# Kernel tuning notes

Measured on AMD Instinct MI355X. Metric: run time of the kernel, lower is better.

## Reference

```python
import jax, jax.numpy as jnp
import numpy as np

B = 64       # number of graphs
R = 148      # fixed ROI count from source
D = 64       # hidden_channels (embed_dim, 4 heads)
H = 4
IN1 = 64     # node feature dim (after stripping label column)
INR = 148    # roi-graph feature dim
HID = 1000
NCLS = 2
N1 = 262144
E1 = 1048576
N2 = B * R
E2 = 262144
EPS = 1e-5


def setup_inputs() -> dict:
    key = jax.random.key(0)
    ks = jax.random.split(key, 40)
    def p(i, shape, s=0.1):
        return jax.random.normal(ks[i], shape, dtype=jnp.float32) * s
    inp = {
        'x_feat': jax.random.normal(ks[0], (N1, IN1), dtype=jnp.float32),
        'node_roi': jax.random.randint(ks[1], (N1,), 0, R, dtype=jnp.int32),
        'batch1': ((jnp.arange(N1, dtype=jnp.int32) * B) // N1).astype(jnp.int32),
        'edge_index1': jax.random.randint(ks[2], (2, E1), 0, N1, dtype=jnp.int32),
        'edge_weight1': jax.random.uniform(ks[3], (E1,), dtype=jnp.float32, minval=0.1, maxval=1.0),
        'x2_feat': jax.random.normal(ks[4], (N2, INR), dtype=jnp.float32),
        'roi_labels2': (jnp.arange(N2, dtype=jnp.int32) % R).astype(jnp.int32),
        'batch2': (jnp.arange(N2, dtype=jnp.int32) // R).astype(jnp.int32),
        'edge_index2': jax.random.randint(ks[5], (2, E2), 0, N2, dtype=jnp.int32),
        'edge_weight2': jax.random.uniform(ks[6], (E2,), dtype=jnp.float32, minval=0.1, maxval=1.0),
        'Wg1': p(7, (IN1, D)), 'bg1': jnp.zeros((D,), jnp.float32),
        'Wg2': p(8, (D, D)), 'bg2': jnp.zeros((D,), jnp.float32),
        'Wr1': p(9, (INR, D)), 'br1': jnp.zeros((D,), jnp.float32),
        'Wr2': p(10, (D, D)), 'br2': jnp.zeros((D,), jnp.float32),
        'in_proj_w': p(11, (3 * D, D)), 'in_proj_b': jnp.zeros((3 * D,), jnp.float32),
        'out_proj_w': p(12, (D, D)), 'out_proj_b': jnp.zeros((D,), jnp.float32),
        'ln1_g': jnp.ones((D,), jnp.float32), 'ln1_b': jnp.zeros((D,), jnp.float32),
        'ff_w1': p(13, (D, D)), 'ff_b1': jnp.zeros((D,), jnp.float32),
        'ff_w2': p(14, (D, D)), 'ff_b2': jnp.zeros((D,), jnp.float32),
        'ln2_g': jnp.ones((D,), jnp.float32), 'ln2_b': jnp.zeros((D,), jnp.float32),
        'Wc1': p(15, (R * D, HID), 0.02), 'bc1': jnp.zeros((HID,), jnp.float32),
        'bn_g': jnp.ones((HID,), jnp.float32), 'bn_b': jnp.zeros((HID,), jnp.float32),
        'Wc2': p(16, (HID, NCLS), 0.02), 'bc2': jnp.zeros((NCLS,), jnp.float32),
    }
    return inp


def gcn_conv(h, src, dst, ew, W, b, n):
    # PyG GCNConv w/ edge weights: add self-loops (weight 1), sym-normalize.
    h = h @ W
    deg = jax.ops.segment_sum(ew, dst, num_segments=n) + 1.0
    dinv = jax.lax.rsqrt(deg)
    norm = dinv[src] * ew * dinv[dst]                      # (E,)
    agg = jax.ops.segment_sum(h[src] * norm[:, None], dst, num_segments=n)
    agg = agg + h * (dinv * dinv)[:, None]                 # self-loop term
    return agg + b


def roi_pool_mean(h, roi, batch):
    # fused scatter mean keyed by (batch, roi) -> (B, R, d); empty slots stay 0
    seg = batch * R + roi
    sums = jax.ops.segment_sum(h, seg, num_segments=B * R)
    cnt = jax.ops.segment_sum(jnp.ones_like(h[:, 0]), seg, num_segments=B * R)
    return (sums / jnp.maximum(cnt, 1.0)[:, None]).reshape(B, R, h.shape[1])


def layer_norm(x, g, b):
    mu = x.mean(axis=-1, keepdims=True)
    var = x.var(axis=-1, keepdims=True)
    return (x - mu) * jax.lax.rsqrt(var + EPS) * g + b


def reference(x_feat, node_roi, batch1, edge_index1, edge_weight1,
              x2_feat, roi_labels2, batch2, edge_index2, edge_weight2,
              Wg1, bg1, Wg2, bg2, Wr1, br1, Wr2, br2,
              in_proj_w, in_proj_b, out_proj_w, out_proj_b,
              ln1_g, ln1_b, ff_w1, ff_b1, ff_w2, ff_b2, ln2_g, ln2_b,
              Wc1, bc1, bn_g, bn_b, Wc2, bc2):
    s1, d1 = edge_index1[0], edge_index1[1]
    s2, d2 = edge_index2[0], edge_index2[1]

    # ROI-graph branch (convs_roi[:-1]): 2 GCN layers, relu, eval dropout=noop
    h2 = jax.nn.relu(gcn_conv(x2_feat, s2, d2, edge_weight2, Wr1, br1, N2))
    h2 = jax.nn.relu(gcn_conv(h2, s2, d2, edge_weight2, Wr2, br2, N2))
    pooled_roi = roi_pool_mean(h2, roi_labels2, batch2)          # (B,R,D)

    # node-graph branch (convs[:-1])
    h1 = jax.nn.relu(gcn_conv(x_feat, s1, d1, edge_weight1, Wg1, bg1, N1))
    h1 = jax.nn.relu(gcn_conv(h1, s1, d1, edge_weight1, Wg2, bg2, N1))
    pooled = roi_pool_mean(h1, node_roi, batch1)                 # (B,R,D)

    combined = pooled + pooled_roi                               # transformer_in_combined

    # SelfAttnBlock (torch MultiheadAttention, batch_first, 4 heads)
    hd = D // H
    qkv = combined @ in_proj_w.T + in_proj_b                     # (B,R,3D)
    q, k, v = jnp.split(qkv, 3, axis=-1)
    q = q.reshape(B, R, H, hd)
    k = k.reshape(B, R, H, hd)
    v = v.reshape(B, R, H, hd)
    scores = jnp.einsum('bqhd,bkhd->bhqk', q, k) / np.sqrt(hd).astype(np.float32)
    attn_w = jax.nn.softmax(scores, axis=-1)                     # (B,H,R,R)
    o = jnp.einsum('bhqk,bkhd->bqhd', attn_w, v).reshape(B, R, D)
    o = o @ out_proj_w.T + out_proj_b
    x = layer_norm(combined + o, ln1_g, ln1_b)
    f = jax.nn.relu(x @ ff_w1 + ff_b1) @ ff_w2 + ff_b2
    t_out = layer_norm(x + f, ln2_g, ln2_b)                      # (B,R,D)

    # classifier: Linear -> BatchNorm1d(eval: mean0,var1) -> LeakyReLU -> Linear
    z = t_out.reshape(B, R * D) @ Wc1 + bc1
    z = bn_g * z * jax.lax.rsqrt(jnp.asarray(1.0 + EPS, z.dtype)) + bn_b
    z = jnp.where(z >= 0, z, 0.01 * z)
    out = z @ Wc2 + bc2                                          # (B,NCLS)
    return (out, pooled, pooled_roi, t_out, attn_w)
```

## Files before the change

kernel.cpp:

```cpp
#include <hip/hip_runtime.h>
#include <cstdint>
#include <cstddef>

#define N1v 262144
#define E1v 1048576
#define N2v 9472
#define E2v 262144
#define BBv 64
#define RRv 148
#define HIDv 1000
#define BRv (BBv * RRv)
#define NSEG 9472
#define EPB 4096
#define NBK1 256
#define SH1 10
#define BINS1 1024
#define CAP1 4864
#define STR1 4608
#define NBK2 74
#define SH2 7
#define BINS2 128
#define CAP2 4096
#define STR2 4096
#define GB1 4096
#define GB2 1184
#define MB1 2048
#define MB2 148
#define PH_B2 (E1v / EPB + E2v / EPB)
#define PH_G1 MB1
#define PH_PC BBv
#define PH_TR 64

__host__ __device__ constexpr int cdiv(int a, int b) { return (a + b - 1) / b; }

typedef __attribute__((ext_vector_type(8))) short bf16x8;
typedef __attribute__((ext_vector_type(4))) float f32x4;
typedef unsigned short ushort_t;
typedef unsigned long long u64;

__device__ inline short f2bf(float f) {
    union { float f; unsigned u; } v; v.f = f;
    unsigned r = v.u + 0x7fff + ((v.u >> 16) & 1);
    return (short)(r >> 16);
}
__device__ inline float bf2f(unsigned hs) {
    union { unsigned u; float f; } v; v.u = hs << 16; return v.f;
}
__device__ inline unsigned relu_pk(unsigned u) {
    unsigned r = u;
    if (r & 0x8000u) r &= 0xFFFF0000u;
    if (r & 0x80000000u) r &= 0x0000FFFFu;
    return r;
}

__device__ inline void binB2_body(const int* __restrict__ src, const int* __restrict__ dst,
                                  const float* __restrict__ ew, int* __restrict__ cur, u64* __restrict__ rb,
                                  int nbk, int sh, int e0, size_t stride,
                                  int* __restrict__ h, int* __restrict__ basg) {
    int tid = threadIdx.x;
    if (tid < nbk) h[tid] = 0;
    __syncthreads();
    for (int t = tid; t < EPB; t += 256) atomicAdd(&h[dst[e0 + t] >> sh], 1);
    __syncthreads();
    if (tid < nbk) {
        int c = h[tid];
        basg[tid] = c ? atomicAdd(&cur[tid], c) : 0;
        h[tid] = 0;
    }
    __syncthreads();
    unsigned lowmask = (1u << sh) - 1u;
    for (int t = tid; t < EPB; t += 256) {
        int d = dst[e0 + t];
        int b = d >> sh;
        int r = atomicAdd(&h[b], 1);
        unsigned lo = ((unsigned)src[e0 + t] << sh) | ((unsigned)d & lowmask);
        rb[(size_t)b * stride + basg[b] + r] = ((u64)(unsigned)__float_as_int(ew[e0 + t]) << 32) | lo;
    }
}

__device__ inline void gemm_f32_body(const float* __restrict__ X, const float* __restrict__ Wmat,
                                     ushort_t* __restrict__ Y, int N, int gw, int tw, int tid) {
    int lane = tid & 63;
    int l15 = lane & 15;
    int lg = lane >> 4;
    bf16x8 bfrag[2][4];
    for (int kh = 0; kh < 2; ++kh)
        for (int ct = 0; ct < 4; ++ct) {
            bf16x8 b;
#pragma unroll
            for (int i = 0; i < 8; ++i)
                b[i] = f2bf(Wmat[(size_t)(kh * 32 + lg * 8 + i) * 64 + ct * 16 + l15]);
            bfrag[kh][ct] = b;
        }
    int ntiles = N >> 4;
    for (int t = gw; t < ntiles; t += tw) {
        int row0 = t << 4;
        const float* xp = X + (size_t)(row0 + l15) * 64 + lg * 8;
        float4 a0 = *(const float4*)(xp);
        float4 a1 = *(const float4*)(xp + 4);
        float4 a2 = *(const float4*)(xp + 32);
        float4 a3 = *(const float4*)(xp + 36);
        bf16x8 af0, af1;
        af0[0] = f2bf(a0.x); af0[1] = f2bf(a0.y); af0[2] = f2bf(a0.z); af0[3] = f2bf(a0.w);
        af0[4] = f2bf(a1.x); af0[5] = f2bf(a1.y); af0[6] = f2bf(a1.z); af0[7] = f2bf(a1.w);
        af1[0] = f2bf(a2.x); af1[1] = f2bf(a2.y); af1[2] = f2bf(a2.z); af1[3] = f2bf(a2.w);
        af1[4] = f2bf(a3.x); af1[5] = f2bf(a3.y); af1[6] = f2bf(a3.z); af1[7] = f2bf(a3.w);
        f32x4 acc0 = {0.f, 0.f, 0.f, 0.f}, acc1 = acc0, acc2 = acc0, acc3 = acc0;
        acc0 = __builtin_amdgcn_mfma_f32_16x16x32_bf16(af0, bfrag[0][0], acc0, 0, 0, 0);
        acc1 = __builtin_amdgcn_mfma_f32_16x16x32_bf16(af0, bfrag[0][1], acc1, 0, 0, 0);
        acc2 = __builtin_amdgcn_mfma_f32_16x16x32_bf16(af0, bfrag[0][2], acc2, 0, 0, 0);
        acc3 = __builtin_amdgcn_mfma_f32_16x16x32_bf16(af0, bfrag[0][3], acc3, 0, 0, 0);
        acc0 = __builtin_amdgcn_mfma_f32_16x16x32_bf16(af1, bfrag[1][0], acc0, 0, 0, 0);
        acc1 = __builtin_amdgcn_mfma_f32_16x16x32_bf16(af1, bfrag[1][1], acc1, 0, 0, 0);
        acc2 = __builtin_amdgcn_mfma_f32_16x16x32_bf16(af1, bfrag[1][2], acc2, 0, 0, 0);
        acc3 = __builtin_amdgcn_mfma_f32_16x16x32_bf16(af1, bfrag[1][3], acc3, 0, 0, 0);
        ushort_t* yp = Y + (size_t)(row0 + lg * 4) * 64 + l15;
#pragma unroll
        for (int r = 0; r < 4; ++r) {
            yp[(size_t)r * 64 + 0]  = (ushort_t)f2bf(acc0[r]);
            yp[(size_t)r * 64 + 16] = (ushort_t)f2bf(acc1[r]);
            yp[(size_t)r * 64 + 32] = (ushort_t)f2bf(acc2[r]);
            yp[(size_t)r * 64 + 48] = (ushort_t)f2bf(acc3[r]);
        }
    }
}

__device__ inline void pool_csr_body(const int* __restrict__ roi, int* __restrict__ offs_p,
                                     int* __restrict__ nodeC, int b, int* __restrict__ smem) {
    int* rl = smem;
    int* hist = smem + 4096;
    int* curs = smem + 4096 + RRv;
    int tid = threadIdx.x;
    for (int t = tid; t < RRv; t += 256) hist[t] = 0;
    __syncthreads();
    int base = b * 4096;
    for (int t = tid; t < 4096; t += 256) {
        int r = roi[base + t];
        rl[t] = r;
        atomicAdd(&hist[r], 1);
    }
    __syncthreads();
    if (tid < RRv) {
        int s = 0;
        for (int k = 0; k < tid; ++k) s += hist[k];
        curs[tid] = s;
        offs_p[b * RRv + tid] = base + s;
    }
    __syncthreads();
    for (int t = tid; t < 4096; t += 256) {
        int r = rl[t];
        int j = atomicAdd(&curs[r], 1);
        nodeC[base + j] = base + t;
    }
}

__global__ __launch_bounds__(256) void k_phase1(
    const int* __restrict__ src1, const int* __restrict__ dst1, const float* __restrict__ ew1,
    int* __restrict__ cur1, u64* __restrict__ rb1,
    const int* __restrict__ src2, const int* __restrict__ dst2, const float* __restrict__ ew2,
    int* __restrict__ cur2, u64* __restrict__ rb2,
    const float* __restrict__ x_feat, const float* __restrict__ Wg1, ushort_t* __restrict__ h1P,
    const int* __restrict__ roi, int* __restrict__ offs_p, int* __restrict__ nodeC,
    const float* __restrict__ Win, float* __restrict__ WinT,
    const float* __restrict__ Wout, float* __restrict__ WoutT) {
    __shared__ int smem[4096 + 2 * RRv];
    int bid = blockIdx.x;
    int tid = threadIdx.x;
    if (bid < PH_B2) {
        if (bid < E1v / EPB)
            binB2_body(src1, dst1, ew1, cur1, rb1, NBK1, SH1, bid * EPB, STR1, smem, smem + 256);
        else
            binB2_body(src2, dst2, ew2, cur2, rb2, NBK2, SH2, (bid - E1v / EPB) * EPB, STR2, smem, smem + 256);
    } else if (bid < PH_B2 + PH_G1) {
        gemm_f32_body(x_feat, Wg1, h1P, N1v, (bid - PH_B2) * 4 + (tid >> 6), PH_G1 * 4, tid);
    } else if (bid < PH_B2 + PH_G1 + PH_PC) {
        pool_csr_body(roi, offs_p, nodeC, bid - PH_B2 - PH_G1, smem);
    } else {
        int i = (bid - PH_B2 - PH_G1 - PH_PC) * 256 + tid;
        if (i < 192 * 64) {
            WinT[(i & 63) * 192 + (i >> 6)] = Win[i];
        } else if (i < 192 * 64 + 64 * 64) {
            int j = i - 192 * 64;
            WoutT[(j & 63) * 64 + (j >> 6)] = Wout[j];
        }
    }
}

__global__ __launch_bounds__(256) void k_scanC(const int* __restrict__ cur1, int* __restrict__ cb1,
                                               const int* __restrict__ cur2, int* __restrict__ cb2) {
    __shared__ int tmp[256];
    int t = threadIdx.x;
    int v = cur1[t];
    tmp[t] = v; __syncthreads();
    int val = v;
    for (int off = 1; off < 256; off <<= 1) { int o = (t >= off) ? tmp[t - off] : 0; __syncthreads(); val += o; tmp[t] = val; __syncthreads(); }
    cb1[t] = val - v;
    if (t == 255) cb1[256] = val;
    __syncthreads();
    int v2 = (t < NBK2) ? cur2[t] : 0;
    tmp[t] = v2; __syncthreads();
    int val2 = v2;
    for (int off = 1; off < 256; off <<= 1) { int o = (t >= off) ? tmp[t - off] : 0; __syncthreads(); val2 += o; tmp[t] = val2; __syncthreads(); }
    if (t < NBK2) cb2[t] = val2 - v2;
    if (t == NBK2 - 1) cb2[NBK2] = val2;
}

template<int BINS, int CAP, int SH, int STRIDE>
__global__ __launch_bounds__(256) void k_csrC(const u64* __restrict__ rb, const int* __restrict__ cnts,
                                              const int* __restrict__ cbase,
                                              float* __restrict__ dinv, int* __restrict__ offs,
                                              int2* __restrict__ snC) {
    int b = blockIdx.x;
    const u64* rbb = rb + (size_t)b * STRIDE;
    int cnt = cnts[b];
    int cb = cbase[b];
    __shared__ int hist[BINS];
    __shared__ float degs[BINS];
    __shared__ int scn[BINS];
    __shared__ int tmp[256];
    extern __shared__ int2 outb[];
    int tid = threadIdx.x;
    for (int i = tid; i < BINS; i += 256) { hist[i] = 0; degs[i] = 0.f; }
    __syncthreads();
    for (int j = tid; j < cnt; j += 256) {
        u64 rec = rbb[j];
        int bin = (int)((unsigned)rec & (BINS - 1));
        float w = __int_as_float((int)(rec >> 32));
        atomicAdd(&hist[bin], 1);
        atomicAdd(&degs[bin], w);
    }
    __syncthreads();
    constexpr int PER = (BINS + 255) / 256;
    int lv[PER];
    int tsum = 0;
    int base_i = tid * PER;
#pragma unroll
    for (int k = 0; k < PER; ++k) { int idx = base_i + k; lv[k] = (idx < BINS) ? hist[idx] : 0; tsum += lv[k]; }
    tmp[tid] = tsum; __syncthreads();
    int val = tsum;
    for (int off = 1; off < 256; off <<= 1) { int o = (tid >= off) ? tmp[tid - off] : 0; __syncthreads(); val += o; tmp[tid] = val; __syncthreads(); }
    int run = val - tsum;
#pragma unroll
    for (int k = 0; k < PER; ++k) { int idx = base_i + k; if (idx < BINS) { scn[idx] = run; run += lv[k]; } }
    __syncthreads();
    for (int i = tid; i < BINS; i += 256) {
        offs[b * BINS + i] = cb + scn[i];
        dinv[b * BINS + i] = rsqrtf(degs[i] + 1.0f);
    }
    __syncthreads();
    bool staged = (cnt <= CAP);
    for (int j = tid; j < cnt; j += 256) {
        u64 rec = rbb[j];
        unsigned lo = (unsigned)rec;
        int bin = (int)(lo & (BINS - 1));
        int s = (int)(lo >> SH);
        float w = __int_as_float((int)(rec >> 32));
        float wd = w * rsqrtf(degs[bin] + 1.0f);
        int r = atomicAdd(&scn[bin], 1);
        int2 o2 = make_int2(s, __float_as_int(wd));
        if (staged) outb[r] = o2;
        else snC[(size_t)cb + r] = o2;
    }
    __syncthreads();
    if (staged) {
        for (int j = tid; j < cnt; j += 256) snC[(size_t)cb + j] = outb[j];
    }
}

__global__ __launch_bounds__(256) void k_normfix(int2* __restrict__ snC1, const float* __restrict__ dinv1,
                                                 int2* __restrict__ snC2, const float* __restrict__ dinv2) {
    int bid = blockIdx.x;
    int2* snC; const float* dinv; int j;
    if (bid < E1v / 256) { snC = snC1; dinv = dinv1; j = bid * 256 + threadIdx.x; }
    else { snC = snC2; dinv = dinv2; j = (bid - E1v / 256) * 256 + threadIdx.x; }
    int2 e = snC[j];
    e.y = __float_as_int(dinv[e.x] * __int_as_float(e.y));
    snC[j] = e;
}

__global__ __launch_bounds__(256) void k_pool_all(const int* __restrict__ nodeC, const int* __restrict__ offs,
                                                  const ushort_t* __restrict__ Ab, const ushort_t* __restrict__ h2Ab,
                                                  float* __restrict__ pooled, float* __restrict__ pooledroi,
                                                  float* __restrict__ comb) {
    int tid = threadIdx.x;
    int lane = tid & 63;
    int nh = lane >> 5;
    int slot = (lane >> 3) & 3;
    int f8 = lane & 7;
    int gw = blockIdx.x * 4 + (tid >> 6);
    int tw = gridDim.x * 4;
    for (int ss = gw * 2; ss < NSEG; ss += tw * 2) {
        int s = ss + nh;
        int beg = offs[s];
        int end = (s + 1 < NSEG) ? offs[s + 1] : N1v;
        float a0 = 0.f, a1 = 0.f, a2 = 0.f, a3 = 0.f, a4 = 0.f, a5 = 0.f, a6 = 0.f, a7 = 0.f;
        for (int j = beg + slot; j < end; j += 4) {
            int node = nodeC[j];
            uint4 v = *(const uint4*)(Ab + (size_t)node * 64 + f8 * 8);
            a0 += fmaxf(bf2f(v.x & 0xffffu), 0.f);
            a1 += fmaxf(bf2f(v.x >> 16), 0.f);
            a2 += fmaxf(bf2f(v.y & 0xffffu), 0.f);
            a3 += fmaxf(bf2f(v.y >> 16), 0.f);
            a4 += fmaxf(bf2f(v.z & 0xffffu), 0.f);
            a5 += fmaxf(bf2f(v.z >> 16), 0.f);
            a6 += fmaxf(bf2f(v.w & 0xffffu), 0.f);
            a7 += fmaxf(bf2f(v.w >> 16), 0.f);
        }
        a0 += __shfl_xor(a0, 8);  a1 += __shfl_xor(a1, 8);  a2 += __shfl_xor(a2, 8);  a3 += __shfl_xor(a3, 8);
        a4 += __shfl_xor(a4, 8);  a5 += __shfl_xor(a5, 8);  a6 += __shfl_xor(a6, 8);  a7 += __shfl_xor(a7, 8);
        a0 += __shfl_xor(a0, 16); a1 += __shfl_xor(a1, 16); a2 += __shfl_xor(a2, 16); a3 += __shfl_xor(a3, 16);
        a4 += __shfl_xor(a4, 16); a5 += __shfl_xor(a5, 16); a6 += __shfl_xor(a6, 16); a7 += __shfl_xor(a7, 16);
        if (slot == 0) {
            float inv = 1.f / (float)max(end - beg, 1);
            float p0 = a0 * inv, p1 = a1 * inv, p2 = a2 * inv, p3 = a3 * inv;
            float p4 = a4 * inv, p5 = a5 * inv, p6 = a6 * inv, p7 = a7 * inv;
            uint4 v2 = *(const uint4*)(h2Ab + (size_t)s * 64 + f8 * 8);
            float q0 = fmaxf(bf2f(v2.x & 0xffffu), 0.f);
            float q1 = fmaxf(bf2f(v2.x >> 16), 0.f);
            float q2 = fmaxf(bf2f(v2.y & 0xffffu), 0.f);
            float q3 = fmaxf(bf2f(v2.y >> 16), 0.f);
            float q4 = fmaxf(bf2f(v2.z & 0xffffu), 0.f);
            float q5 = fmaxf(bf2f(v2.z >> 16), 0.f);
            float q6 = fmaxf(bf2f(v2.w & 0xffffu), 0.f);
            float q7 = fmaxf(bf2f(v2.w >> 16), 0.f);
            size_t bo = (size_t)s * 64 + f8 * 8;
            float4 t;
            t.x = p0; t.y = p1; t.z = p2; t.w = p3; *(float4*)(pooled + bo) = t;
            t.x = p4; t.y = p5; t.z = p6; t.w = p7; *(float4*)(pooled + bo + 4) = t;
            t.x = q0; t.y = q1; t.z = q2; t.w = q3; *(float4*)(pooledroi + bo) = t;
            t.x = q4; t.y = q5; t.z = q6; t.w = q7; *(float4*)(pooledroi + bo + 4) = t;
            t.x = p0 + q0; t.y = p1 + q1; t.z = p2 + q2; t.w = p3 + q3; *(float4*)(comb + bo) = t;
            t.x = p4 + q4; t.y = p5 + q5; t.z = p6 + q6; t.w = p7 + q7; *(float4*)(comb + bo + 4) = t;
        }
    }
}

__device__ inline void gather_body(const int2* __restrict__ snC, const int* __restrict__ offs,
                                   const ushort_t* __restrict__ Pb, const float* __restrict__ dinv,
                                   const float* __restrict__ bias, ushort_t* __restrict__ A,
                                   int N, int E, int gw, int tw, int lane) {
    int nh = lane >> 5;
    int slot = (lane >> 3) & 3;
    int f8 = lane & 7;
    float4 bv0 = *(const float4*)(bias + f8 * 8);
    float4 bv1 = *(const float4*)(bias + f8 * 8 + 4);
    for (int ii = gw * 2; ii < N; ii += tw * 2) {
        int i = ii + nh;
        int beg = offs[i];
        int end = (i + 1 < N) ? offs[i + 1] : E;
        float a0 = 0.f, a1 = 0.f, a2 = 0.f, a3 = 0.f, a4 = 0.f, a5 = 0.f, a6 = 0.f, a7 = 0.f;
        for (int j = beg + slot; j < end; j += 4) {
            int2 e = snC[j];
            int s = e.x;
            float nv = __int_as_float(e.y);
            uint4 w = *(const uint4*)(Pb + (size_t)s * 64 + f8 * 8);
            a0 = fmaf(nv, bf2f(w.x & 0xffffu), a0);
            a1 = fmaf(nv, bf2f(w.x >> 16), a1);
            a2 = fmaf(nv, bf2f(w.y & 0xffffu), a2);
            a3 = fmaf(nv, bf2f(w.y >> 16), a3);
            a4 = fmaf(nv, bf2f(w.z & 0xffffu), a4);
            a5 = fmaf(nv, bf2f(w.z >> 16), a5);
            a6 = fmaf(nv, bf2f(w.w & 0xffffu), a6);
            a7 = fmaf(nv, bf2f(w.w >> 16), a7);
        }
        a0 += __shfl_xor(a0, 8);  a1 += __shfl_xor(a1, 8);  a2 += __shfl_xor(a2, 8);  a3 += __shfl_xor(a3, 8);
        a4 += __shfl_xor(a4, 8);  a5 += __shfl_xor(a5, 8);  a6 += __shfl_xor(a6, 8);  a7 += __shfl_xor(a7, 8);
        a0 += __shfl_xor(a0, 16); a1 += __shfl_xor(a1, 16); a2 += __shfl_xor(a2, 16); a3 += __shfl_xor(a3, 16);
        a4 += __shfl_xor(a4, 16); a5 += __shfl_xor(a5, 16); a6 += __shfl_xor(a6, 16); a7 += __shfl_xor(a7, 16);
        if (slot == 0) {
            uint4 w = *(const uint4*)(Pb + (size_t)i * 64 + f8 * 8);
            float di = dinv[i];
            float s2 = di * di;
            float r0 = fmaf(s2, bf2f(w.x & 0xffffu), a0) + bv0.x;
            float r1 = fmaf(s2, bf2f(w.x >> 16),    a1) + bv0.y;
            float r2 = fmaf(s2, bf2f(w.y & 0xffffu), a2) + bv0.z;
            float r3 = fmaf(s2, bf2f(w.y >> 16),    a3) + bv0.w;
            float r4 = fmaf(s2, bf2f(w.z & 0xffffu), a4) + bv1.x;
            float r5 = fmaf(s2, bf2f(w.z >> 16),    a5) + bv1.y;
            float r6 = fmaf(s2, bf2f(w.w & 0xffffu), a6) + bv1.z;
            float r7 = fmaf(s2, bf2f(w.w >> 16),    a7) + bv1.w;
            uint4 ov;
            ov.x = (unsigned)(ushort_t)f2bf(r0) | ((unsigned)(ushort_t)f2bf(r1) << 16);
            ov.y = (unsigned)(ushort_t)f2bf(r2) | ((unsigned)(ushort_t)f2bf(r3) << 16);
            ov.z = (unsigned)(ushort_t)f2bf(r4) | ((unsigned)(ushort_t)f2bf(r5) << 16);
            ov.w = (unsigned)(ushort_t)f2bf(r6) | ((unsigned)(ushort_t)f2bf(r7) << 16);
            *(uint4*)(A + (size_t)i * 64 + f8 * 8) = ov;
        }
    }
}

__global__ __launch_bounds__(256) void k_gather_both(const int2* __restrict__ snC1, const int* __restrict__ offs1,
                                                     const ushort_t* __restrict__ P1, const float* __restrict__ dinv1,
                                                     const float* __restrict__ b1, ushort_t* __restrict__ A1,
                                                     const int2* __restrict__ snC2, const int* __restrict__ offs2,
                                                     const ushort_t* __restrict__ P2, const float* __restrict__ dinv2,
                                                     const float* __restrict__ b2, ushort_t* __restrict__ A2) {
    int tid = threadIdx.x;
    int lane = tid & 63;
    if (blockIdx.x < GB1)
        gather_body(snC1, offs1, P1, dinv1, b1, A1, N1v, E1v,
                    blockIdx.x * 4 + (tid >> 6), GB1 * 4, lane);
    else
        gather_body(snC2, offs2, P2, dinv2, b2, A2, N2v, E2v,
                    (blockIdx.x - GB1) * 4 + (tid >> 6), GB2 * 4, lane);
}

__device__ inline void gemm_bf16_body(const ushort_t* __restrict__ X, const float* __restrict__ Wmat,
                                      ushort_t* __restrict__ Y, int N, int gw, int tw, int tid) {
    int lane = tid & 63;
    int l15 = lane & 15;
    int lg = lane >> 4;
    bf16x8 bfrag[2][4];
    for (int kh = 0; kh < 2; ++kh)
        for (int ct = 0; ct < 4; ++ct) {
            bf16x8 b;
#pragma unroll
            for (int i = 0; i < 8; ++i)
                b[i] = f2bf(Wmat[(size_t)(kh * 32 + lg * 8 + i) * 64 + ct * 16 + l15]);
            bfrag[kh][ct] = b;
        }
    int ntiles = N >> 4;
    for (int t = gw; t < ntiles; t += tw) {
        int row0 = t << 4;
        const ushort_t* xp = X + (size_t)(row0 + l15) * 64 + lg * 8;
        uint4 c0 = *(const uint4*)(xp);
        uint4 c1 = *(const uint4*)(xp + 32);
        c0.x = relu_pk(c0.x); c0.y = relu_pk(c0.y); c0.z = relu_pk(c0.z); c0.w = relu_pk(c0.w);
        c1.x = relu_pk(c1.x); c1.y = relu_pk(c1.y); c1.z = relu_pk(c1.z); c1.w = relu_pk(c1.w);
        bf16x8 af0 = *reinterpret_cast<bf16x8*>(&c0);
        bf16x8 af1 = *reinterpret_cast<bf16x8*>(&c1);
        f32x4 acc0 = {0.f, 0.f, 0.f, 0.f}, acc1 = acc0, acc2 = acc0, acc3 = acc0;
        acc0 = __builtin_amdgcn_mfma_f32_16x16x32_bf16(af0, bfrag[0][0], acc0, 0, 0, 0);
        acc1 = __builtin_amdgcn_mfma_f32_16x16x32_bf16(af0, bfrag[0][1], acc1, 0, 0, 0);
        acc2 = __builtin_amdgcn_mfma_f32_16x16x32_bf16(af0, bfrag[0][2], acc2, 0, 0, 0);
        acc3 = __builtin_amdgcn_mfma_f32_16x16x32_bf16(af0, bfrag[0][3], acc3, 0, 0, 0);
        acc0 = __builtin_amdgcn_mfma_f32_16x16x32_bf16(af1, bfrag[1][0], acc0, 0, 0, 0);
        acc1 = __builtin_amdgcn_mfma_f32_16x16x32_bf16(af1, bfrag[1][1], acc1, 0, 0, 0);
        acc2 = __builtin_amdgcn_mfma_f32_16x16x32_bf16(af1, bfrag[1][2], acc2, 0, 0, 0);
        acc3 = __builtin_amdgcn_mfma_f32_16x16x32_bf16(af1, bfrag[1][3], acc3, 0, 0, 0);
        ushort_t* yp = Y + (size_t)(row0 + lg * 4) * 64 + l15;
#pragma unroll
        for (int r = 0; r < 4; ++r) {
            yp[(size_t)r * 64 + 0]  = (ushort_t)f2bf(acc0[r]);
            yp[(size_t)r * 64 + 16] = (ushort_t)f2bf(acc1[r]);
            yp[(size_t)r * 64 + 32] = (ushort_t)f2bf(acc2[r]);
            yp[(size_t)r * 64 + 48] = (ushort_t)f2bf(acc3[r]);
        }
    }
}

__global__ __launch_bounds__(256) void k_gemm_both(const ushort_t* __restrict__ X1, const float* __restrict__ W1,
                                                   ushort_t* __restrict__ Y1,
                                                   const ushort_t* __restrict__ X2, const float* __restrict__ W2,
                                                   ushort_t* __restrict__ Y2) {
    int tid = threadIdx.x;
    if (blockIdx.x < MB1)
        gemm_bf16_body(X1, W1, Y1, N1v, blockIdx.x * 4 + (tid >> 6), MB1 * 4, tid);
    else
        gemm_bf16_body(X2, W2, Y2, N2v, (blockIdx.x - MB1) * 4 + (tid >> 6), MB2 * 4, tid);
}

template<int MB, bool RIN, bool ROUT, bool OBF16>
__global__ __launch_bounds__(256) void k_gemm_rowwave(const float* __restrict__ X, const float* __restrict__ W,
                                                      const float* __restrict__ bias, void* __restrict__ Yv,
                                                      int N, int K) {
    extern __shared__ float Wl[];
    const int M = MB * 64;
    for (int idx = threadIdx.x; idx < K * M; idx += 256) Wl[idx] = W[idx];
    __syncthreads();
    int lane = threadIdx.x & 63;
    int gw = blockIdx.x * 4 + (threadIdx.x >> 6);
    int tw = gridDim.x * 4;
    const int K4 = K >> 2;
    for (int row = gw; row < N; row += tw) {
        float acc[MB];
#pragma unroll
        for (int cb = 0; cb < MB; ++cb) acc[cb] = 0.f;
        const float4* xr = (const float4*)(X + (size_t)row * K);
        for (int k4 = 0; k4 < K4; ++k4) {
            float4 xv = xr[k4];
            if (RIN) {
                xv.x = fmaxf(xv.x, 0.f); xv.y = fmaxf(xv.y, 0.f);
                xv.z = fmaxf(xv.z, 0.f); xv.w = fmaxf(xv.w, 0.f);
            }
            const float* wp = Wl + (k4 * 4) * M + lane;
#pragma unroll
            for (int cb = 0; cb < MB; ++cb) acc[cb] = fmaf(xv.x, wp[cb * 64], acc[cb]);
            wp += M;
#pragma unroll
            for (int cb = 0; cb < MB; ++cb) acc[cb] = fmaf(xv.y, wp[cb * 64], acc[cb]);
            wp += M;
#pragma unroll
            for (int cb = 0; cb < MB; ++cb) acc[cb] = fmaf(xv.z, wp[cb * 64], acc[cb]);
            wp += M;
#pragma unroll
            for (int cb = 0; cb < MB; ++cb) acc[cb] = fmaf(xv.w, wp[cb * 64], acc[cb]);
        }
#pragma unroll
        for (int cb = 0; cb < MB; ++cb) {
            float y = acc[cb];
            int col = cb * 64 + lane;
            if (bias) y += bias[col];
            if (ROUT) y = fmaxf(y, 0.f);
            if (OBF16) ((ushort_t*)Yv)[(size_t)row * M + col] = (ushort_t)f2bf(y);
            else ((float*)Yv)[(size_t)row * M + col] = y;
        }
    }
}

__global__ __launch_bounds__(256) void k_attn(const float* __restrict__ qkv, float* __restrict__ aw,
                                              float* __restrict__ o) {
    int qc = blockIdx.x & 3;
    int bh = blockIdx.x >> 2;
    int b = bh >> 2, h = bh & 3;
    __shared__ float qs[37][16];
    __shared__ float kT[16][152];
    __shared__ float vs[148][16];
    __shared__ float ps[4][152];
    int tid = threadIdx.x;
    const float* base = qkv + (size_t)b * 148 * 192 + h * 16;
    for (int idx = tid; idx < 148 * 16; idx += 256) {
        int i = idx >> 4, d = idx & 15;
        const float* p = base + (size_t)i * 192 + d;
        kT[d][i] = p[64];
        vs[i][d] = p[128];
    }
    int q0 = qc * 37;
    for (int idx = tid; idx < 37 * 16; idx += 256) {
        int i = idx >> 4, d = idx & 15;
        qs[i][d] = base[(size_t)(q0 + i) * 192 + d] * 0.25f;
    }
    __syncthreads();
    int wv = tid >> 6, lane = tid & 63;
    float* aw_bh = aw + (size_t)bh * 148 * 148;
    for (int ii = wv; ii < 37; ii += 4) {
        int i = q0 + ii;
        float s0 = 0.f, s1 = 0.f, s2 = 0.f;
#pragma unroll
        for (int d = 0; d < 16; ++d) {
            float q = qs[ii][d];
            s0 = fmaf(q, kT[d][lane], s0);
            s1 = fmaf(q, kT[d][lane + 64], s1);
            if (lane < 20) s2 = fmaf(q, kT[d][lane + 128], s2);
        }
        float m = fmaxf(s0, s1);
        if (lane < 20) m = fmaxf(m, s2);
#pragma unroll
        for (int off = 1; off < 64; off <<= 1) m = fmaxf(m, __shfl_xor(m, off));
        float e0 = __expf(s0 - m), e1 = __expf(s1 - m);
        float e2 = (lane < 20) ? __expf(s2 - m) : 0.f;
        float sum = e0 + e1 + e2;
#pragma unroll
        for (int off = 1; off < 64; off <<= 1) sum += __shfl_xor(sum, off);
        float inv = 1.f / sum;
        float p0 = e0 * inv, p1 = e1 * inv, p2 = e2 * inv;
        float* awr = aw_bh + (size_t)i * 148;
        awr[lane] = p0;
        awr[lane + 64] = p1;
        if (lane < 20) awr[lane + 128] = p2;
        ps[wv][lane] = p0;
        ps[wv][lane + 64] = p1;
        if (lane < 20) ps[wv][lane + 128] = p2;
        int d = lane & 15, jj = lane >> 4;
        float acc = 0.f;
        for (int t = jj; t < 148; t += 4) acc = fmaf(ps[wv][t], vs[t][d], acc);
        acc += __shfl_xor(acc, 16);
        acc += __shfl_xor(acc, 32);
        if (lane < 16) o[((size_t)b * 148 + i) * 64 + h * 16 + d] = acc;
    }
}

__global__ __launch_bounds__(256) void k_ln_gemm(const float* __restrict__ X, const float* __restrict__ Wt,
                                                 const float* __restrict__ bias, const float* __restrict__ resid,
                                                 const float* __restrict__ g, const float* __restrict__ bb,
                                                 float* __restrict__ Y, int N) {
    __shared__ float Wl[4096];
    for (int idx = threadIdx.x; idx < 4096; idx += 256) Wl[idx] = Wt[idx];
    __syncthreads();
    int lane = threadIdx.x & 63;
    int gw = blockIdx.x * 4 + (threadIdx.x >> 6);
    int tw = gridDim.x * 4;
    for (int row = gw; row < N; row += tw) {
        const float4* xr = (const float4*)(X + (size_t)row * 64);
        float acc = 0.f;
        for (int k4 = 0; k4 < 16; ++k4) {
            float4 xv = xr[k4];
            const float* wp = Wl + (k4 * 4) * 64 + lane;
            acc = fmaf(xv.x, wp[0], acc);
            acc = fmaf(xv.y, wp[64], acc);
            acc = fmaf(xv.z, wp[128], acc);
            acc = fmaf(xv.w, wp[192], acc);
        }
        float y = acc + bias[lane] + resid[(size_t)row * 64 + lane];
        float s = y;
#pragma unroll
        for (int off = 1; off < 64; off <<= 1) s += __shfl_xor(s, off);
        float mu = s * (1.f / 64.f);
        float dcen = y - mu;
        float v = dcen * dcen;
#pragma unroll
        for (int off = 1; off < 64; off <<= 1) v += __shfl_xor(v, off);
        float var = v * (1.f / 64.f);
        Y[(size_t)row * 64 + lane] = dcen * rsqrtf(var + 1e-5f) * g[lane] + bb[lane];
    }
}

__global__ __launch_bounds__(256) void k_cls_part(const float* __restrict__ T, const float* __restrict__ Wc1,
                                                  float* __restrict__ Zp) {
    int ks = blockIdx.x >> 2;
    int mt = blockIdx.x & 3;
    int k0 = ks * 74;
    int m0 = mt * 256;
    __shared__ float Tl[64][74];
    int tid = threadIdx.x;
    for (int idx = tid; idx < 64 * 74; idx += 256) {
        int b = idx / 74, kk = idx - b * 74;
        Tl[b][kk] = T[(size_t)b * 9472 + k0 + kk];
    }
    __syncthreads();
    int lane = tid & 63, bq = tid >> 6;
    int mbase = m0 + lane * 4;
    size_t moff = (mbase + 3 < 1000) ? (size_t)mbase : 0;
    float4 acc[16];
#pragma unroll
    for (int j = 0; j < 16; ++j) acc[j] = make_float4(0.f, 0.f, 0.f, 0.f);
#pragma unroll 2
    for (int kk = 0; kk < 74; ++kk) {
        float4 w = *(const float4*)(Wc1 + (size_t)(k0 + kk) * 1000 + moff);
#pragma unroll
        for (int j = 0; j < 16; ++j) {
            float t = Tl[bq * 16 + j][kk];
            acc[j].x = fmaf(t, w.x, acc[j].x);
            acc[j].y = fmaf(t, w.y, acc[j].y);
            acc[j].z = fmaf(t, w.z, acc[j].z);
            acc[j].w = fmaf(t, w.w, acc[j].w);
        }
    }
    float* zp = Zp + (size_t)ks * 64 * 1024;
#pragma unroll
    for (int j = 0; j < 16; ++j) {
        int b = bq * 16 + j;
        *(float4*)(zp + (size_t)b * 1024 + mbase) = acc[j];
    }
}

__global__ __launch_bounds__(256) void k_cls_reduce(const float* __restrict__ Zp, const float* __restrict__ bc1,
                                                    const float* __restrict__ bn_g, const float* __restrict__ bn_b,
                                                    float* __restrict__ zb) {
    int flat = blockIdx.x * 256 + threadIdx.x;
    int b = flat >> 10, m = flat & 1023;
    if (m >= 1000) return;
    float s = 0.f;
    for (int ks = 0; ks < 128; ++ks)
        s += Zp[((size_t)ks * 64 + b) * 1024 + m];
    float rs = rsqrtf(1.0f + 1e-5f);
    float z = bn_g[m] * (s + bc1[m]) * rs + bn_b[m];
    zb[flat] = z >= 0.f ? z : 0.01f * z;
}

__global__ __launch_bounds__(256) void k_cls_final(const float* __restrict__ zb,
                                                   const float* __restrict__ Wc2, const float* __restrict__ bc2,
                                                   float* __restrict__ out) {
    int b = blockIdx.x;
    int tid = threadIdx.x;
    float a0 = 0.f, a1 = 0.f;
    for (int m = tid; m < 1000; m += 256) {
        float z = zb[b * 1024 + m];
        a0 = fmaf(z, Wc2[m * 2], a0);
        a1 = fmaf(z, Wc2[m * 2 + 1], a1);
    }
#pragma unroll
    for (int off = 1; off < 64; off <<= 1) {
        a0 += __shfl_xor(a0, off);
        a1 += __shfl_xor(a1, off);
    }
    __shared__ float r0[4], r1[4];
    if ((tid & 63) == 0) { r0[tid >> 6] = a0; r1[tid >> 6] = a1; }
    __syncthreads();
    if (tid == 0) {
        out[b * 2 + 0] = r0[0] + r0[1] + r0[2] + r0[3] + bc2[0];
        out[b * 2 + 1] = r1[0] + r1[1] + r1[2] + r1[3] + bc2[1];
    }
}

extern "C" void kernel_launch(void* const* d_in, const int* in_sizes, int n_in,
                              void* d_out, int out_size, void* d_ws, size_t ws_size,
                              hipStream_t stream) {
    (void)in_sizes; (void)n_in; (void)out_size; (void)ws_size;

    const float* x_feat = (const float*)d_in[0];
    const int* node_roi = (const int*)d_in[1];
    const int* ei1 = (const int*)d_in[3];
    const float* ew1 = (const float*)d_in[4];
    const float* x2f = (const float*)d_in[5];
    const int* ei2 = (const int*)d_in[8];
    const float* ew2 = (const float*)d_in[9];
    const float* Wg1 = (const float*)d_in[10];
    const float* bg1 = (const float*)d_in[11];
    const float* Wg2 = (const float*)d_in[12];
    const float* bg2 = (const float*)d_in[13];
    const float* Wr1 = (const float*)d_in[14];
    const float* br1 = (const float*)d_in[15];
    const float* Wr2 = (const float*)d_in[16];
    const float* br2 = (const float*)d_in[17];
    const float* in_proj_w = (const float*)d_in[18];
    const float* in_proj_b = (const float*)d_in[19];
    const float* out_proj_w = (const float*)d_in[20];
    const float* out_proj_b = (const float*)d_in[21];
    const float* ln1_g = (const float*)d_in[22];
    const float* ln1_b = (const float*)d_in[23];
    const float* ff_w1 = (const float*)d_in[24];
    const float* ff_b1 = (const float*)d_in[25];
    const float* ff_w2 = (const float*)d_in[26];
    const float* ff_b2 = (const float*)d_in[27];
    const float* ln2_g = (const float*)d_in[28];
    const float* ln2_b = (const float*)d_in[29];
    const float* Wc1 = (const float*)d_in[30];
    const float* bc1 = (const float*)d_in[31];
    const float* bn_g = (const float*)d_in[32];
    const float* bn_b = (const float*)d_in[33];
    const float* Wc2 = (const float*)d_in[34];
    const float* bc2 = (const float*)d_in[35];

    const int* src1 = ei1;
    const int* dst1 = ei1 + E1v;
    const int* src2 = ei2;
    const int* dst2 = ei2 + E2v;

    float* out = (float*)d_out;
    const int PSZ = BRv * 64;
    float* pooled_out = out + 128;
    float* pooledroi_out = out + 128 + PSZ;
    float* tout_out = out + 128 + 2 * PSZ;
    float* attn_out = out + 128 + 3 * PSZ;

    float* W = (float*)d_ws;
    size_t o = 0;
    int* cur1 = (int*)(W + o); o += 256;
    int* cur2 = (int*)(W + o); o += 128;
    size_t zone_elems = o;
    int* cb1 = (int*)(W + o);  o += 260;
    int* cb2 = (int*)(W + o);  o += 76;
    o = (o + 1) & ~(size_t)1;
    u64* rb1 = (u64*)(W + o);  o += (size_t)NBK1 * STR1 * 2;
    u64* rb2 = (u64*)(W + o);  o += (size_t)NBK2 * STR2 * 2;
    int2* snC1 = (int2*)(W + o); o += (size_t)E1v * 2;
    int2* snC2 = (int2*)(W + o); o += (size_t)E2v * 2;
    float* dinv1 = W + o;        o += N1v;
    float* dinv2 = W + o;        o += N2v;
    int* offs1 = (int*)(W + o);  o += N1v;
    int* offs2 = (int*)(W + o);  o += N2v;
    int* offs_p = (int*)(W + o); o += NSEG;
    int* nodeC = (int*)(W + o);  o += N1v;
    float* zbuf = W + o;         o += BBv * 1024;
    float* WinT = W + o;  o += 192 * 64;
    float* WoutT = W + o; o += 64 * 64;
    o = (o + 1) & ~(size_t)1;
    ushort_t* h2P = (ushort_t*)(W + o);  o += (size_t)N2v * 32;
    ushort_t* h2Ab = (ushort_t*)(W + o); o += (size_t)N2v * 32;
    o = (o + 1) & ~(size_t)1;
    size_t h1P_off = o; o += (size_t)N1v * 64;
    size_t h1A_off = o; o += (size_t)N1v * 64;
    ushort_t* h1P = (ushort_t*)(W + h1P_off);
    ushort_t* h1Ab = (ushort_t*)(W + h1A_off);
    size_t p = h1P_off;
    float* comb = W + p; p += PSZ;
    float* qkvb = W + p; p += (size_t)BRv * 192;
    float* obuf = W + p; p += PSZ;
    float* xbuf = W + p; p += PSZ;
    float* f1 = W + p;   p += PSZ;
    float* Zp = W + h1A_off;

    dim3 blk(256);

    hipMemsetAsync(W, 0, zone_elems * sizeof(float), stream);

    k_phase1<<<PH_B2 + PH_G1 + PH_PC + PH_TR, blk, 0, stream>>>(
        src1, dst1, ew1, cur1, rb1, src2, dst2, ew2, cur2, rb2,
        x_feat, Wg1, h1P, node_roi, offs_p, nodeC,
        in_proj_w, WinT, out_proj_w, WoutT);
    k_gemm_rowwave<1, false, false, true><<<cdiv(N2v, 4), blk, 148 * 64 * 4, stream>>>(x2f, Wr1, nullptr, h2P, N2v, 148);
    k_scanC<<<1, blk, 0, stream>>>(cur1, cb1, cur2, cb2);
    k_csrC<BINS1, CAP1, SH1, STR1><<<NBK1, blk, CAP1 * 8, stream>>>(rb1, cur1, cb1, dinv1, offs1, snC1);
    k_csrC<BINS2, CAP2, SH2, STR2><<<NBK2, blk, CAP2 * 8, stream>>>(rb2, cur2, cb2, dinv2, offs2, snC2);
    k_normfix<<<E1v / 256 + E2v / 256, blk, 0, stream>>>(snC1, dinv1, snC2, dinv2);

    k_gather_both<<<GB1 + GB2, blk, 0, stream>>>(snC1, offs1, h1P, dinv1, bg1, h1Ab,
                                                 snC2, offs2, h2P, dinv2, br1, h2Ab);
    k_gemm_both<<<MB1 + MB2, blk, 0, stream>>>(h1Ab, Wg2, h1P, h2Ab, Wr2, h2P);
    k_gather_both<<<GB1 + GB2, blk, 0, stream>>>(snC1, offs1, h1P, dinv1, bg2, h1Ab,
                                                 snC2, offs2, h2P, dinv2, br2, h2Ab);
    k_pool_all<<<2048, blk, 0, stream>>>(nodeC, offs_p, h1Ab, h2Ab, pooled_out, pooledroi_out, comb);

    k_gemm_rowwave<3, false, false, false><<<cdiv(N2v, 4), blk, 64 * 192 * 4, stream>>>(comb, WinT, in_proj_b, qkvb, N2v, 64);
    k_attn<<<BBv * 4 * 4, blk, 0, stream>>>(qkvb, attn_out, obuf);
    k_ln_gemm<<<cdiv(N2v, 4), blk, 0, stream>>>(obuf, WoutT, out_proj_b, comb, ln1_g, ln1_b, xbuf, N2v);
    k_gemm_rowwave<1, false, true, false><<<cdiv(N2v, 4), blk, 64 * 64 * 4, stream>>>(xbuf, ff_w1, ff_b1, f1, N2v, 64);
    k_ln_gemm<<<cdiv(N2v, 4), blk, 0, stream>>>(f1, ff_w2, ff_b2, xbuf, ln2_g, ln2_b, tout_out, N2v);

    k_cls_part<<<512, blk, 0, stream>>>(tout_out, Wc1, Zp);
    k_cls_reduce<<<BBv * 1024 / 256, blk, 0, stream>>>(Zp, bc1, bn_g, bn_b, zbuf);
    k_cls_final<<<BBv, blk, 0, stream>>>(zbuf, Wc2, bc2, out);
}
```

Baseline: 390.5 us.

## Halve edge-binning block size and store classifier partial sums as bf16

The edge-binning phase now processes 2048 edges per block instead of 4096, which doubles the number of binning blocks in the fused phase-1 kernel and gives more parallelism with shorter per-block loops. Separately, the classifier's split-K partial sums are written as bf16 rather than fp32, which halves the write and read traffic of the 128-way partial buffer in the reduce kernel. The bf16 partials lose precision before the 128-term sum, which risks exceeding output tolerance. More blocks also mean more global atomics on the bucket cursors.

```diff
diff --git a/kernel.cpp b/kernel.cpp
--- a/kernel.cpp
+++ b/kernel.cpp
@@ -11,7 +11,7 @@
 #define HIDv 1000
 #define BRv (BBv * RRv)
 #define NSEG 9472
-#define EPB 4096
+#define EPBB 2048
 #define NBK1 256
 #define SH1 10
 #define BINS1 1024
@@ -26,7 +26,7 @@
 #define GB2 1184
 #define MB1 2048
 #define MB2 148
-#define PH_B2 (E1v / EPB + E2v / EPB)
+#define PH_B2 (E1v / EPBB + E2v / EPBB)
 #define PH_G1 MB1
 #define PH_PC BBv
 #define PH_TR 64
@@ -60,7 +60,7 @@
     int tid = threadIdx.x;
     if (tid < nbk) h[tid] = 0;
     __syncthreads();
-    for (int t = tid; t < EPB; t += 256) atomicAdd(&h[dst[e0 + t] >> sh], 1);
+    for (int t = tid; t < EPBB; t += 256) atomicAdd(&h[dst[e0 + t] >> sh], 1);
     __syncthreads();
     if (tid < nbk) {
         int c = h[tid];
@@ -69,7 +69,7 @@
     }
     __syncthreads();
     unsigned lowmask = (1u << sh) - 1u;
-    for (int t = tid; t < EPB; t += 256) {
+    for (int t = tid; t < EPBB; t += 256) {
         int d = dst[e0 + t];
         int b = d >> sh;
         int r = atomicAdd(&h[b], 1);
@@ -167,10 +167,10 @@
     int bid = blockIdx.x;
     int tid = threadIdx.x;
     if (bid < PH_B2) {
-        if (bid < E1v / EPB)
-            binB2_body(src1, dst1, ew1, cur1, rb1, NBK1, SH1, bid * EPB, STR1, smem, smem + 256);
+        if (bid < E1v / EPBB)
+            binB2_body(src1, dst1, ew1, cur1, rb1, NBK1, SH1, bid * EPBB, STR1, smem, smem + 256);
         else
-            binB2_body(src2, dst2, ew2, cur2, rb2, NBK2, SH2, (bid - E1v / EPB) * EPB, STR2, smem, smem + 256);
+            binB2_body(src2, dst2, ew2, cur2, rb2, NBK2, SH2, (bid - E1v / EPBB) * EPBB, STR2, smem, smem + 256);
     } else if (bid < PH_B2 + PH_G1) {
         gemm_f32_body(x_feat, Wg1, h1P, N1v, (bid - PH_B2) * 4 + (tid >> 6), PH_G1 * 4, tid);
     } else if (bid < PH_B2 + PH_G1 + PH_PC) {
@@ -606,7 +606,7 @@
 }
 
 __global__ __launch_bounds__(256) void k_cls_part(const float* __restrict__ T, const float* __restrict__ Wc1,
-                                                  float* __restrict__ Zp) {
+                                                  ushort_t* __restrict__ Zp) {
     int ks = blockIdx.x >> 2;
     int mt = blockIdx.x & 3;
     int k0 = ks * 74;
@@ -636,15 +636,20 @@
             acc[j].w = fmaf(t, w.w, acc[j].w);
         }
     }
-    float* zp = Zp + (size_t)ks * 64 * 1024;
+    ushort_t* zp = Zp + (size_t)ks * 64 * 1024;
 #pragma unroll
     for (int j = 0; j < 16; ++j) {
         int b = bq * 16 + j;
-        *(float4*)(zp + (size_t)b * 1024 + mbase) = acc[j];
-    }
-}
-
-__global__ __launch_bounds__(256) void k_cls_reduce(const float* __restrict__ Zp, const float* __restrict__ bc1,
+        ushort4 pk;
+        pk.x = (ushort_t)f2bf(acc[j].x);
+        pk.y = (ushort_t)f2bf(acc[j].y);
+        pk.z = (ushort_t)f2bf(acc[j].z);
+        pk.w = (ushort_t)f2bf(acc[j].w);
+        *(ushort4*)(zp + (size_t)b * 1024 + mbase) = pk;
+    }
+}
+
+__global__ __launch_bounds__(256) void k_cls_reduce(const ushort_t* __restrict__ Zp, const float* __restrict__ bc1,
                                                     const float* __restrict__ bn_g, const float* __restrict__ bn_b,
                                                     float* __restrict__ zb) {
     int flat = blockIdx.x * 256 + threadIdx.x;
@@ -652,7 +657,7 @@
     if (m >= 1000) return;
     float s = 0.f;
     for (int ks = 0; ks < 128; ++ks)
-        s += Zp[((size_t)ks * 64 + b) * 1024 + m];
+        s += bf2f(Zp[((size_t)ks * 64 + b) * 1024 + m]);
     float rs = rsqrtf(1.0f + 1e-5f);
     float z = bn_g[m] * (s + bc1[m]) * rs + bn_b[m];
     zb[flat] = z >= 0.f ? z : 0.01f * z;
@@ -769,7 +774,7 @@
     float* obuf = W + p; p += PSZ;
     float* xbuf = W + p; p += PSZ;
     float* f1 = W + p;   p += PSZ;
-    float* Zp = W + h1A_off;
+    ushort_t* Zp = (ushort_t*)(W + h1A_off);
 
     dim3 blk(256);
 
```

New measurement: 399.6 us. +2.3%, slower.
